# Kernel optimization log

Measured on AMD Instinct MI355X. Metric: run time of the kernel, lower is better.

Reference implementation:

```python
import math
import jax, jax.numpy as jnp
import numpy as np

NUM_HEADS = 12
NUM_LANDMARKS = 32

def iterative_inv(mat, n_iter=6):
    # mat: [B, H, m, m] row-stochastic kernel; Newton-Schulz pseudo-inverse
    m = mat.shape[-1]
    I = jnp.eye(m, dtype=mat.dtype)
    K = mat
    # 'else' branch: per-(B,H) normalization by max column sum
    denom = jnp.max(jnp.sum(K, axis=-2), axis=-1)[..., None, None]
    V = jnp.swapaxes(K, -1, -2) / denom
    for _ in range(n_iter):
        KV = jnp.matmul(K, V)
        V = jnp.matmul(0.25 * V, 13.0 * I - jnp.matmul(KV, 15.0 * I - jnp.matmul(KV, 7.0 * I - KV)))
    return V

def setup_inputs() -> dict:
    key = jax.random.key(0)
    k1, k2, k3 = jax.random.split(key, 3)
    B, N, C = 8, 2048, 768
    x = jax.random.normal(k1, (B, N, C), dtype=jnp.float32)
    w_qkv = jax.random.normal(k2, (C, 3 * C), dtype=jnp.float32) * (1.0 / math.sqrt(C))
    w_proj = jax.random.normal(k3, (C, C), dtype=jnp.float32) * (1.0 / math.sqrt(C))
    b_proj = jnp.zeros((C,), dtype=jnp.float32)
    return {"x": x, "w_qkv": w_qkv, "w_proj": w_proj, "b_proj": b_proj}

def reference(x, w_qkv, w_proj, b_proj):
    B, N, C = x.shape
    H = NUM_HEADS
    d = C // H
    m = NUM_LANDMARKS
    qkv = (x @ w_qkv).reshape(B, N, 3, H, d).transpose(2, 0, 3, 1, 4)  # [3,B,H,N,d]
    Q, K, V = qkv[0], qkv[1], qkv[2]
    scale = 1.0 / math.sqrt(math.sqrt(d))
    Q = Q * scale
    K = K * scale
    # landmark pooling: mean over contiguous chunks of size N//m
    Q_l = Q.reshape(B, H, m, N // m, d).mean(axis=-2)  # [B,H,m,d]
    K_l = K.reshape(B, H, m, N // m, d).mean(axis=-2)
    kernel_1 = jax.nn.softmax(jnp.einsum('bhnd,bhmd->bhnm', Q, K_l), axis=-1)   # [B,H,N,m]
    kernel_2 = jax.nn.softmax(jnp.einsum('bhmd,bhkd->bhmk', Q_l, K_l), axis=-1) # [B,H,m,m]
    kernel_3 = jax.nn.softmax(jnp.einsum('bhmd,bhnd->bhmn', Q_l, K), axis=-1)   # [B,H,m,N]
    X = jnp.matmul(jnp.matmul(kernel_1, iterative_inv(kernel_2)), jnp.matmul(kernel_3, V))  # [B,H,N,d]
    X = X.transpose(0, 2, 1, 3).reshape(B, N, C)
    return X @ w_proj + b_proj
```

## Files before the change

### kernel.cpp

```cpp
#include <hip/hip_runtime.h>
#include <hip/hip_bf16.h>

typedef __hip_bfloat16 bf16;
typedef __attribute__((ext_vector_type(8))) __bf16 bf16x8;
typedef __attribute__((ext_vector_type(4))) float f32x4;

#define NB 8
#define SEQ 2048
#define CH 768
#define NH 12
#define HD 64
#define NL 32
#define BHT (NB*NH)
#define TOK (NB*SEQ)
#define QK_SCALE 0.35355339059327379f

__device__ __forceinline__ void async_ld16(const bf16* g, bf16* l) {
    unsigned loff = (unsigned)__builtin_amdgcn_readfirstlane((int)(unsigned)(uintptr_t)l);
    __builtin_amdgcn_global_load_lds(
        (const __attribute__((address_space(1))) unsigned*)(uintptr_t)g,
        (__attribute__((address_space(3))) unsigned*)(uintptr_t)loff, 16, 0, 0);
}

__global__ void convert_x(const float* __restrict__ x, bf16* __restrict__ xb) {
    size_t i = ((size_t)blockIdx.x * 256 + threadIdx.x) * 8;
    float4 a = *reinterpret_cast<const float4*>(x + i);
    float4 b = *reinterpret_cast<const float4*>(x + i + 4);
    alignas(16) bf16 tmp[8];
    tmp[0] = __float2bfloat16(a.x); tmp[1] = __float2bfloat16(a.y);
    tmp[2] = __float2bfloat16(a.z); tmp[3] = __float2bfloat16(a.w);
    tmp[4] = __float2bfloat16(b.x); tmp[5] = __float2bfloat16(b.y);
    tmp[6] = __float2bfloat16(b.z); tmp[7] = __float2bfloat16(b.w);
    *reinterpret_cast<uint4*>(xb + i) = *reinterpret_cast<const uint4*>(tmp);
}

__global__ void transpose_f32(const float* __restrict__ in, bf16* __restrict__ outp,
                              int Hrows, int Wcols) {
    __shared__ float tile[32][33];
    int bx = blockIdx.x * 32, by = blockIdx.y * 32;
    int tx = threadIdx.x, ty = threadIdx.y;
    for (int i = 0; i < 32; i += 8)
        tile[ty + i][tx] = in[(size_t)(by + ty + i) * Wcols + bx + tx];
    __syncthreads();
    for (int i = 0; i < 32; i += 8)
        outp[(size_t)(bx + ty + i) * Hrows + by + tx] = __float2bfloat16(tile[tx][ty + i]);
}

template <int EPI>
__global__ __launch_bounds__(256) void gemm_bt(
    const bf16* __restrict__ A, const bf16* __restrict__ Bt,
    int Nout, int Kdim,
    bf16* __restrict__ q, bf16* __restrict__ k, bf16* __restrict__ vt,
    float* __restrict__ Ql, float* __restrict__ Kl,
    float* __restrict__ outp, const float* __restrict__ bias_f) {
    __shared__ __align__(16) bf16 As[128 * 32];
    __shared__ __align__(16) bf16 Bs[128 * 32];
    const int t = threadIdx.x;
    const int wave = t >> 6, lane = t & 63;
    const int quad = lane >> 4, l15 = lane & 15;
    const int wr = wave >> 1, wc = wave & 1;

    int p = blockIdx.y * gridDim.x + blockIdx.x;
    int xcd = p & 7, j = p >> 3;
    int gx = gridDim.x;
    int bn = j % gx;
    int bm = (j / gx) * 8 + xcd;
    const int bm0 = bm * 128;
    const int bn0 = bn * 128;

    f32x4 acc[4][4];
    const f32x4 zero4 = {0.f, 0.f, 0.f, 0.f};
    for (int i = 0; i < 4; i++)
        for (int jj = 0; jj < 4; jj++) acc[i][jj] = zero4;

    const int sw = (quad ^ (l15 & 3)) * 8;

    for (int k0 = 0; k0 < Kdim; k0 += 32) {
        __syncthreads();
        #pragma unroll
        for (int r = 0; r < 2; r++) {
            int c = t + r * 256;
            int row = c >> 2;
            int chunk = ((c & 3) ^ (row & 3)) * 8;
            async_ld16(&A[(size_t)(bm0 + row) * Kdim + k0 + chunk], &As[(wave * 64 + r * 256) * 8]);
            async_ld16(&Bt[(size_t)(bn0 + row) * Kdim + k0 + chunk], &Bs[(wave * 64 + r * 256) * 8]);
        }
        __syncthreads();
        bf16x8 af[4], bfr[4];
        #pragma unroll
        for (int mi = 0; mi < 4; mi++)
            af[mi] = *reinterpret_cast<const bf16x8*>(&As[(wr * 64 + mi * 16 + l15) * 32 + sw]);
        #pragma unroll
        for (int ni = 0; ni < 4; ni++)
            bfr[ni] = *reinterpret_cast<const bf16x8*>(&Bs[(wc * 64 + ni * 16 + l15) * 32 + sw]);
        #pragma unroll
        for (int mi = 0; mi < 4; mi++)
            #pragma unroll
            for (int ni = 0; ni < 4; ni++)
                acc[mi][ni] = __builtin_amdgcn_mfma_f32_16x16x32_bf16(af[mi], bfr[ni], acc[mi][ni], 0, 0, 0);
    }

    if (EPI == 0) {
        const int which = bn0 / CH;
        const int rem0 = bn0 - which * CH + wc * 64;
        const int b = bm0 >> 11;
        const int nnb = (bm0 & 2047) + wr * 64;
        if (which < 2) {
            bf16* dstqk = (which == 0) ? q : k;
            float* dstl = (which == 0) ? Ql : Kl;
            const int l = nnb >> 6;
            #pragma unroll
            for (int ni = 0; ni < 4; ni++) {
                int rem = rem0 + ni * 16 + l15;
                int h = rem >> 6, dd = rem & 63;
                int bh = b * NH + h;
                float colsum = 0.f;
                #pragma unroll
                for (int mi = 0; mi < 4; mi++) {
                    int nn0 = nnb + mi * 16 + quad * 4;
                    #pragma unroll
                    for (int r = 0; r < 4; r++) {
                        float val = acc[mi][ni][r];
                        colsum += val;
                        dstqk[((size_t)bh * SEQ + nn0 + r) * HD + dd] = __float2bfloat16(val * QK_SCALE);
                    }
                }
                colsum += __shfl_xor(colsum, 16);
                colsum += __shfl_xor(colsum, 32);
                if (quad == 0)
                    dstl[((size_t)bh * NL + l) * HD + dd] = colsum * (QK_SCALE / 64.f);
            }
        } else {
            #pragma unroll
            for (int ni = 0; ni < 4; ni++) {
                int rem = rem0 + ni * 16 + l15;
                int h = rem >> 6, dd = rem & 63;
                int bh = b * NH + h;
                #pragma unroll
                for (int mi = 0; mi < 4; mi++) {
                    int nn0 = nnb + mi * 16 + quad * 4;
                    alignas(8) bf16 four[4];
                    #pragma unroll
                    for (int r = 0; r < 4; r++) four[r] = __float2bfloat16(acc[mi][ni][r]);
                    *reinterpret_cast<uint2*>(&vt[((size_t)bh * HD + dd) * SEQ + nn0]) =
                        *reinterpret_cast<const uint2*>(four);
                }
            }
        }
    } else {
        #pragma unroll
        for (int mi = 0; mi < 4; mi++)
            #pragma unroll
            for (int ni = 0; ni < 4; ni++) {
                int col = bn0 + wc * 64 + ni * 16 + l15;
                #pragma unroll
                for (int r = 0; r < 4; r++) {
                    int row = bm0 + wr * 64 + mi * 16 + quad * 4 + r;
                    outp[(size_t)row * Nout + col] = acc[mi][ni][r] + bias_f[col];
                }
            }
    }
}

__global__ __launch_bounds__(256) void k3_pv(const float* __restrict__ Ql,
                                             const bf16* __restrict__ Kb,
                                             const bf16* __restrict__ Vt,
                                             float* __restrict__ Opart,
                                             float* __restrict__ Spart) {
    __shared__ __align__(16) bf16 Pw[4][32 * 136];
    __shared__ __align__(16) float Ored[4][32 * 65];
    __shared__ float Sred[4 * 32];
    const int bh = blockIdx.x, cc = blockIdx.y;
    const int n0 = cc * 512;
    const int t = threadIdx.x;
    const int w = t >> 6, lane = t & 63;
    const int quad = lane >> 4, l15 = lane & 15;

    const bf16* Kbh = Kb + (size_t)bh * SEQ * HD;
    const bf16* Vtb = Vt + (size_t)bh * HD * SEQ;

    bf16x8 af[2][2];
    #pragma unroll
    for (int mt = 0; mt < 2; mt++)
        #pragma unroll
        for (int kh = 0; kh < 2; kh++) {
            const float* src = Ql + (size_t)bh * NL * HD + (mt * 16 + l15) * 64 + kh * 32 + quad * 8;
            alignas(16) bf16 tmp[8];
            #pragma unroll
            for (int jj = 0; jj < 8; jj++) tmp[jj] = __float2bfloat16(src[jj]);
            af[mt][kh] = *reinterpret_cast<const bf16x8*>(tmp);
        }

    const f32x4 zero4 = {0.f, 0.f, 0.f, 0.f};
    f32x4 oacc[2][4];
    #pragma unroll
    for (int mt = 0; mt < 2; mt++)
        #pragma unroll
        for (int nd = 0; nd < 4; nd++) oacc[mt][nd] = zero4;
    float rs[2][4];
    #pragma unroll
    for (int mt = 0; mt < 2; mt++)
        #pragma unroll
        for (int r = 0; r < 4; r++) rs[mt][r] = 0.f;

    bf16* Pme = &Pw[w][0];

    #pragma unroll
    for (int h = 0; h < 2; h++) {
        f32x4 sacc[2][4];
        #pragma unroll
        for (int mt = 0; mt < 2; mt++)
            #pragma unroll
            for (int nt = 0; nt < 4; nt++) sacc[mt][nt] = zero4;
        #pragma unroll
        for (int nt = 0; nt < 4; nt++) {
            int n = n0 + w * 128 + h * 64 + nt * 16 + l15;
            bf16x8 kf0 = *reinterpret_cast<const bf16x8*>(&Kbh[(size_t)n * HD + quad * 8]);
            bf16x8 kf1 = *reinterpret_cast<const bf16x8*>(&Kbh[(size_t)n * HD + 32 + quad * 8]);
            #pragma unroll
            for (int mt = 0; mt < 2; mt++) {
                sacc[mt][nt] = __builtin_amdgcn_mfma_f32_16x16x32_bf16(af[mt][0], kf0, sacc[mt][nt], 0, 0, 0);
                sacc[mt][nt] = __builtin_amdgcn_mfma_f32_16x16x32_bf16(af[mt][1], kf1, sacc[mt][nt], 0, 0, 0);
            }
        }
        #pragma unroll
        for (int mt = 0; mt < 2; mt++)
            #pragma unroll
            for (int nt = 0; nt < 4; nt++)
                #pragma unroll
                for (int r = 0; r < 4; r++) {
                    float pv = __expf(sacc[mt][nt][r]);
                    rs[mt][r] += pv;
                    int row = mt * 16 + quad * 4 + r;
                    Pme[row * 136 + h * 64 + nt * 16 + l15] = __float2bfloat16(pv);
                }
    }
    __asm__ __volatile__("s_waitcnt lgkmcnt(0)" ::: "memory");

    #pragma unroll
    for (int kt = 0; kt < 4; kt++) {
        bf16x8 pa[2];
        pa[0] = *reinterpret_cast<const bf16x8*>(&Pme[l15 * 136 + kt * 32 + quad * 8]);
        pa[1] = *reinterpret_cast<const bf16x8*>(&Pme[(16 + l15) * 136 + kt * 32 + quad * 8]);
        int kbase = n0 + w * 128 + kt * 32 + quad * 8;
        #pragma unroll
        for (int nd = 0; nd < 4; nd++) {
            bf16x8 bv = *reinterpret_cast<const bf16x8*>(&Vtb[(size_t)(nd * 16 + l15) * SEQ + kbase]);
            oacc[0][nd] = __builtin_amdgcn_mfma_f32_16x16x32_bf16(pa[0], bv, oacc[0][nd], 0, 0, 0);
            oacc[1][nd] = __builtin_amdgcn_mfma_f32_16x16x32_bf16(pa[1], bv, oacc[1][nd], 0, 0, 0);
        }
    }

    #pragma unroll
    for (int mt = 0; mt < 2; mt++)
        #pragma unroll
        for (int r = 0; r < 4; r++) {
            float v = rs[mt][r];
            #pragma unroll
            for (int o = 1; o < 16; o <<= 1) v += __shfl_xor(v, o);
            rs[mt][r] = v;
        }
    if (l15 == 0)
        #pragma unroll
        for (int mt = 0; mt < 2; mt++)
            #pragma unroll
            for (int r = 0; r < 4; r++)
                Sred[w * 32 + mt * 16 + quad * 4 + r] = rs[mt][r];
    #pragma unroll
    for (int mt = 0; mt < 2; mt++)
        #pragma unroll
        for (int nd = 0; nd < 4; nd++)
            #pragma unroll
            for (int r = 0; r < 4; r++)
                Ored[w][(mt * 16 + quad * 4 + r) * 65 + nd * 16 + l15] = oacc[mt][nd][r];
    __syncthreads();

    float* Op = Opart + ((size_t)bh * 4 + cc) * (NL * HD);
    for (int e = t; e < 2048; e += 256) {
        int m = e >> 6, dd = e & 63;
        Op[e] = Ored[0][m * 65 + dd] + Ored[1][m * 65 + dd] +
                Ored[2][m * 65 + dd] + Ored[3][m * 65 + dd];
    }
    if (t < 32)
        Spart[((size_t)bh * 4 + cc) * NL + t] = Sred[t] + Sred[32 + t] + Sred[64 + t] + Sred[96 + t];
}

__device__ inline void mm32(float* Cm, const float* Am, const float* Bm, int t) {
    for (int e = t; e < 1024; e += 256) {
        int i = e >> 5, jj = e & 31;
        float s = 0.f;
        #pragma unroll
        for (int kk = 0; kk < 32; kk++) s += Am[i * 32 + kk] * Bm[kk * 32 + jj];
        Cm[e] = s;
    }
}

__global__ __launch_bounds__(256) void newton_inv(const float* __restrict__ Ql,
                                                  const float* __restrict__ Kl,
                                                  const float* __restrict__ Opart,
                                                  const float* __restrict__ Spart,
                                                  float* __restrict__ W2) {
    __shared__ float K2[1024], Vv[1024], KV[1024], Ta[1024], Tb[1024];
    __shared__ float K3[2048];
    __shared__ float stot[32];
    __shared__ float red[32];
    __shared__ float denom_s;
    int bh = blockIdx.x;
    int t = threadIdx.x;
    const float* ql = Ql + (size_t)bh * NL * HD;
    const float* kl = Kl + (size_t)bh * NL * HD;

    if (t < 32) {
        const float* sp = Spart + (size_t)bh * 4 * NL;
        stot[t] = sp[t] + sp[32 + t] + sp[64 + t] + sp[96 + t];
    }
    {
        const float* op = Opart + (size_t)bh * 4 * (NL * HD);
        for (int e = t; e < 2048; e += 256)
            K3[e] = op[e] + op[2048 + e] + op[4096 + e] + op[6144 + e];
    }

    for (int e = t; e < 1024; e += 256) {
        int i = e >> 5, jj = e & 31;
        float s = 0.f;
        #pragma unroll 8
        for (int d = 0; d < 64; d++) s += ql[i * 64 + d] * kl[jj * 64 + d];
        K2[e] = s;
    }
    __syncthreads();
    for (int e = t; e < 2048; e += 256) K3[e] *= (1.f / stot[e >> 6]);
    if (t < 32) {
        float mx = -1e30f;
        for (int jj = 0; jj < 32; jj++) mx = fmaxf(mx, K2[t * 32 + jj]);
        float sm = 0.f;
        for (int jj = 0; jj < 32; jj++) { float e = __expf(K2[t * 32 + jj] - mx); K2[t * 32 + jj] = e; sm += e; }
        float inv = 1.f / sm;
        for (int jj = 0; jj < 32; jj++) K2[t * 32 + jj] *= inv;
    }
    __syncthreads();
    if (t < 32) {
        float cs = 0.f;
        for (int i = 0; i < 32; i++) cs += K2[i * 32 + t];
        red[t] = cs;
    }
    __syncthreads();
    if (t == 0) {
        float mx = red[0];
        for (int jj = 1; jj < 32; jj++) mx = fmaxf(mx, red[jj]);
        denom_s = mx;
    }
    __syncthreads();
    float invden = 1.f / denom_s;
    for (int e = t; e < 1024; e += 256) {
        int i = e >> 5, jj = e & 31;
        Vv[e] = K2[jj * 32 + i] * invden;
    }
    __syncthreads();
    for (int it = 0; it < 6; it++) {
        mm32(KV, K2, Vv, t);
        __syncthreads();
        for (int e = t; e < 1024; e += 256) { int i = e >> 5, jj = e & 31; Ta[e] = ((i == jj) ? 7.f : 0.f) - KV[e]; }
        __syncthreads();
        mm32(Tb, KV, Ta, t);
        __syncthreads();
        for (int e = t; e < 1024; e += 256) { int i = e >> 5, jj = e & 31; Tb[e] = ((i == jj) ? 15.f : 0.f) - Tb[e]; }
        __syncthreads();
        mm32(Ta, KV, Tb, t);
        __syncthreads();
        for (int e = t; e < 1024; e += 256) { int i = e >> 5, jj = e & 31; Ta[e] = ((i == jj) ? 13.f : 0.f) - Ta[e]; }
        __syncthreads();
        mm32(Tb, Vv, Ta, t);
        __syncthreads();
        for (int e = t; e < 1024; e += 256) Vv[e] = 0.25f * Tb[e];
        __syncthreads();
    }
    for (int e = t; e < 2048; e += 256) {
        int i = e >> 6, dd = e & 63;
        float s = 0.f;
        #pragma unroll
        for (int kk = 0; kk < 32; kk++) s += Vv[i * 32 + kk] * K3[kk * 64 + dd];
        W2[(size_t)bh * NL * HD + e] = s;
    }
}

__global__ __launch_bounds__(256) void rows_fused(const bf16* __restrict__ Qb,
                                                  const float* __restrict__ Kl,
                                                  const float* __restrict__ W2,
                                                  bf16* __restrict__ Xp) {
    __shared__ __align__(16) bf16 Klb[32 * 64];
    __shared__ __align__(16) bf16 W2t[64 * 32];
    __shared__ __align__(16) bf16 Pw[4][32 * 40];
    const int bh = blockIdx.x, tile = blockIdx.y;
    const int t = threadIdx.x, w = t >> 6, lane = t & 63;
    const int quad = lane >> 4, l15 = lane & 15;

    {
        const float* ksrc = Kl + (size_t)bh * NL * HD;
        const float* wsrc = W2 + (size_t)bh * NL * HD;
        int e0 = t * 8;
        #pragma unroll
        for (int jj = 0; jj < 8; jj++) {
            int e = e0 + jj;
            Klb[e] = __float2bfloat16(ksrc[e]);
            int kk = e >> 6, dd = e & 63;
            W2t[dd * 32 + kk] = __float2bfloat16(wsrc[e]);
        }
    }
    __syncthreads();

    const int b = bh / NH, h = bh - b * NH;
    const int row0 = tile * 128 + w * 32;
    const bf16* qbase = Qb + ((size_t)bh * SEQ + row0) * HD;

    const f32x4 zero4 = {0.f, 0.f, 0.f, 0.f};
    f32x4 sacc[2][2];
    #pragma unroll
    for (int mt = 0; mt < 2; mt++)
        #pragma unroll
        for (int nt = 0; nt < 2; nt++) sacc[mt][nt] = zero4;
    #pragma unroll
    for (int kh = 0; kh < 2; kh++) {
        bf16x8 bk0 = *reinterpret_cast<const bf16x8*>(&Klb[(l15) * 64 + kh * 32 + quad * 8]);
        bf16x8 bk1 = *reinterpret_cast<const bf16x8*>(&Klb[(16 + l15) * 64 + kh * 32 + quad * 8]);
        #pragma unroll
        for (int mt = 0; mt < 2; mt++) {
            bf16x8 aq = *reinterpret_cast<const bf16x8*>(&qbase[(size_t)(mt * 16 + l15) * HD + kh * 32 + quad * 8]);
            sacc[mt][0] = __builtin_amdgcn_mfma_f32_16x16x32_bf16(aq, bk0, sacc[mt][0], 0, 0, 0);
            sacc[mt][1] = __builtin_amdgcn_mfma_f32_16x16x32_bf16(aq, bk1, sacc[mt][1], 0, 0, 0);
        }
    }

    float invs[2][4];
    bf16* Pme = &Pw[w][0];
    #pragma unroll
    for (int mt = 0; mt < 2; mt++)
        #pragma unroll
        for (int r = 0; r < 4; r++) {
            float v0 = __expf(sacc[mt][0][r]);
            float v1 = __expf(sacc[mt][1][r]);
            int row = mt * 16 + quad * 4 + r;
            Pme[row * 40 + l15] = __float2bfloat16(v0);
            Pme[row * 40 + 16 + l15] = __float2bfloat16(v1);
            float v = v0 + v1;
            #pragma unroll
            for (int o = 1; o < 16; o <<= 1) v += __shfl_xor(v, o);
            invs[mt][r] = 1.f / v;
        }
    __asm__ __volatile__("s_waitcnt lgkmcnt(0)" ::: "memory");

    f32x4 oacc[2][4];
    #pragma unroll
    for (int mt = 0; mt < 2; mt++)
        #pragma unroll
        for (int nd = 0; nd < 4; nd++) oacc[mt][nd] = zero4;
    bf16x8 pa[2];
    pa[0] = *reinterpret_cast<const bf16x8*>(&Pme[l15 * 40 + quad * 8]);
    pa[1] = *reinterpret_cast<const bf16x8*>(&Pme[(16 + l15) * 40 + quad * 8]);
    #pragma unroll
    for (int nd = 0; nd < 4; nd++) {
        bf16x8 bw = *reinterpret_cast<const bf16x8*>(&W2t[(nd * 16 + l15) * 32 + quad * 8]);
        oacc[0][nd] = __builtin_amdgcn_mfma_f32_16x16x32_bf16(pa[0], bw, oacc[0][nd], 0, 0, 0);
        oacc[1][nd] = __builtin_amdgcn_mfma_f32_16x16x32_bf16(pa[1], bw, oacc[1][nd], 0, 0, 0);
    }

    #pragma unroll
    for (int mt = 0; mt < 2; mt++)
        #pragma unroll
        for (int nd = 0; nd < 4; nd++)
            #pragma unroll
            for (int r = 0; r < 4; r++) {
                int row = row0 + mt * 16 + quad * 4 + r;
                Xp[((size_t)(b * SEQ + row)) * CH + h * 64 + nd * 16 + l15] =
                    __float2bfloat16(oacc[mt][nd][r] * invs[mt][r]);
            }
}

extern "C" void kernel_launch(void* const* d_in, const int* in_sizes, int n_in,
                              void* d_out, int out_size, void* d_ws, size_t ws_size,
                              hipStream_t stream) {
    const float* x      = (const float*)d_in[0];
    const float* w_qkv  = (const float*)d_in[1];
    const float* w_proj = (const float*)d_in[2];
    const float* b_proj = (const float*)d_in[3];
    float* out = (float*)d_out;

    char* ws = (char*)d_ws;
    size_t off = 0;
    auto alloc = [&](size_t bytes) -> void* {
        void* p = ws + off;
        off += (bytes + 255) & ~(size_t)255;
        return p;
    };
    bf16* wqkvT  = (bf16*)alloc((size_t)3 * CH * CH * 2);
    bf16* wprojT = (bf16*)alloc((size_t)CH * CH * 2);
    bf16* Qb     = (bf16*)alloc((size_t)BHT * SEQ * HD * 2);
    bf16* Kb     = (bf16*)alloc((size_t)BHT * SEQ * HD * 2);
    bf16* Vt     = (bf16*)alloc((size_t)BHT * SEQ * HD * 2);
    float* Ql    = (float*)alloc((size_t)BHT * NL * HD * 4);
    float* Kl    = (float*)alloc((size_t)BHT * NL * HD * 4);
    float* Opart = (float*)alloc((size_t)BHT * 4 * NL * HD * 4);
    float* Spart = (float*)alloc((size_t)BHT * 4 * NL * 4);
    float* W2    = (float*)alloc((size_t)BHT * NL * HD * 4);
    bf16* Xp     = (bf16*)alloc((size_t)TOK * CH * 2);
    if (ws_size < off) return;
    bf16* xb = Xp;

    convert_x<<<TOK * CH / 2048, 256, 0, stream>>>(x, xb);
    transpose_f32<<<dim3((3 * CH) / 32, CH / 32), dim3(32, 8), 0, stream>>>(w_qkv, wqkvT, CH, 3 * CH);
    transpose_f32<<<dim3(CH / 32, CH / 32), dim3(32, 8), 0, stream>>>(w_proj, wprojT, CH, CH);

    gemm_bt<0><<<dim3((3 * CH) / 128, TOK / 128), 256, 0, stream>>>(
        xb, wqkvT, 3 * CH, CH, Qb, Kb, Vt, Ql, Kl, nullptr, nullptr);

    k3_pv<<<dim3(BHT, 4), 256, 0, stream>>>(Ql, Kb, Vt, Opart, Spart);
    newton_inv<<<BHT, 256, 0, stream>>>(Ql, Kl, Opart, Spart, W2);
    rows_fused<<<dim3(BHT, SEQ / 128), 256, 0, stream>>>(Qb, Kl, W2, Xp);

    gemm_bt<1><<<dim3(CH / 128, TOK / 128), 256, 0, stream>>>(
        Xp, wprojT, CH, CH, nullptr, nullptr, nullptr, nullptr, nullptr, out, b_proj);
}
```

Before: 283.2 us.

## Stage V-transpose epilogue through LDS and drop swizzle and XCD block remap

```diff
diff --git a/kernel.cpp b/kernel.cpp
--- a/kernel.cpp
+++ b/kernel.cpp
@@ -53,46 +53,39 @@
     bf16* __restrict__ q, bf16* __restrict__ k, bf16* __restrict__ vt,
     float* __restrict__ Ql, float* __restrict__ Kl,
     float* __restrict__ outp, const float* __restrict__ bias_f) {
-    __shared__ __align__(16) bf16 As[128 * 32];
-    __shared__ __align__(16) bf16 Bs[128 * 32];
+    __shared__ __align__(16) char smem[EPI == 0 ? 34816 : 16384];
+    bf16* As = (bf16*)smem;
+    bf16* Bs = (bf16*)(smem + 8192);
     const int t = threadIdx.x;
     const int wave = t >> 6, lane = t & 63;
     const int quad = lane >> 4, l15 = lane & 15;
     const int wr = wave >> 1, wc = wave & 1;
-
-    int p = blockIdx.y * gridDim.x + blockIdx.x;
-    int xcd = p & 7, j = p >> 3;
-    int gx = gridDim.x;
-    int bn = j % gx;
-    int bm = (j / gx) * 8 + xcd;
-    const int bm0 = bm * 128;
-    const int bn0 = bn * 128;
+    const int bm0 = blockIdx.y * 128;
+    const int bn0 = blockIdx.x * 128;
 
     f32x4 acc[4][4];
     const f32x4 zero4 = {0.f, 0.f, 0.f, 0.f};
     for (int i = 0; i < 4; i++)
         for (int jj = 0; jj < 4; jj++) acc[i][jj] = zero4;
 
-    const int sw = (quad ^ (l15 & 3)) * 8;
-
     for (int k0 = 0; k0 < Kdim; k0 += 32) {
         __syncthreads();
         #pragma unroll
         for (int r = 0; r < 2; r++) {
             int c = t + r * 256;
             int row = c >> 2;
-            int chunk = ((c & 3) ^ (row & 3)) * 8;
-            async_ld16(&A[(size_t)(bm0 + row) * Kdim + k0 + chunk], &As[(wave * 64 + r * 256) * 8]);
-            async_ld16(&Bt[(size_t)(bn0 + row) * Kdim + k0 + chunk], &Bs[(wave * 64 + r * 256) * 8]);
+            int col = (c & 3) * 8;
+            async_ld16(&A[(size_t)(bm0 + row) * Kdim + k0 + col], &As[(wave * 64 + r * 256) * 8]);
+            async_ld16(&Bt[(size_t)(bn0 + row) * Kdim + k0 + col], &Bs[(wave * 64 + r * 256) * 8]);
         }
         __syncthreads();
         bf16x8 af[4], bfr[4];
         #pragma unroll
         for (int mi = 0; mi < 4; mi++)
-            af[mi] = *reinterpret_cast<const bf16x8*>(&As[(wr * 64 + mi * 16 + l15) * 32 + sw]);
+            af[mi] = *reinterpret_cast<const bf16x8*>(&As[(wr * 64 + mi * 16 + l15) * 32 + quad * 8]);
         #pragma unroll
         for (int ni = 0; ni < 4; ni++)
-            bfr[ni] = *reinterpret_cast<const bf16x8*>(&Bs[(wc * 64 + ni * 16 + l15) * 32 + sw]);
+            bfr[ni] = *reinterpret_cast<const bf16x8*>(&Bs[(wc * 64 + ni * 16 + l15) * 32 + quad * 8]);
         #pragma unroll
         for (int mi = 0; mi < 4; mi++)
             #pragma unroll
@@ -102,12 +95,13 @@
 
     if (EPI == 0) {
         const int which = bn0 / CH;
-        const int rem0 = bn0 - which * CH + wc * 64;
         const int b = bm0 >> 11;
-        const int nnb = (bm0 & 2047) + wr * 64;
+        const int nstart = bm0 & 2047;
         if (which < 2) {
             bf16* dstqk = (which == 0) ? q : k;
             float* dstl = (which == 0) ? Ql : Kl;
+            const int rem0 = bn0 - which * CH + wc * 64;
+            const int nnb = nstart + wr * 64;
             const int l = nnb >> 6;
             #pragma unroll
             for (int ni = 0; ni < 4; ni++) {
@@ -131,20 +125,31 @@
                     dstl[((size_t)bh * NL + l) * HD + dd] = colsum * (QK_SCALE / 64.f);
             }
         } else {
+            __syncthreads();
+            bf16* VT = (bf16*)smem;
             #pragma unroll
             for (int ni = 0; ni < 4; ni++) {
-                int rem = rem0 + ni * 16 + l15;
-                int h = rem >> 6, dd = rem & 63;
-                int bh = b * NH + h;
+                int colL = wc * 64 + ni * 16 + l15;
                 #pragma unroll
                 for (int mi = 0; mi < 4; mi++) {
-                    int nn0 = nnb + mi * 16 + quad * 4;
+                    int nn = wr * 64 + mi * 16 + quad * 4;
                     alignas(8) bf16 four[4];
                     #pragma unroll
                     for (int r = 0; r < 4; r++) four[r] = __float2bfloat16(acc[mi][ni][r]);
-                    *reinterpret_cast<uint2*>(&vt[((size_t)bh * HD + dd) * SEQ + nn0]) =
+                    *reinterpret_cast<uint2*>(&VT[colL * 136 + nn]) =
                         *reinterpret_cast<const uint2*>(four);
                 }
+            }
+            __syncthreads();
+            const int rem0c = bn0 - 2 * CH;
+            #pragma unroll
+            for (int pass = 0; pass < 8; pass++) {
+                int rowL = (t >> 4) + pass * 16;
+                int h = (rem0c + rowL) >> 6, dd = rowL & 63;
+                int bh = b * NH + h;
+                int off = (t & 15) * 8;
+                uint4 val = *reinterpret_cast<const uint4*>(&VT[rowL * 136 + off]);
+                *reinterpret_cast<uint4*>(&vt[((size_t)bh * HD + dd) * SEQ + nstart + off]) = val;
             }
         }
     } else {
```

After: 294.1 us. 3.9% more time.
